# Performance work log

Measured on AMD Instinct MI355X. Metric: run time of the kernel, lower is better.

The kernel has to match this reference:

```python
import jax, jax.numpy as jnp
import numpy as np

GROUP = 128

def _dequant(q, s, z):
    # q: [O, K] int4 values in [0,16); s,z: [O, K//GROUP]
    O, K = q.shape
    qg = q.reshape(O, K // GROUP, GROUP)
    w = (qg - z[:, :, None]).astype(s.dtype) * s[:, :, None]
    return w.reshape(O, K)

def setup_inputs() -> dict:
    key = jax.random.key(0)
    ks = jax.random.split(key, 7)
    H, I = 4096, 14336
    x = jax.random.normal(ks[0], (2, 2048, H), jnp.float32)
    q_up = jax.random.randint(ks[1], (I, H), 0, 16, jnp.int32)
    s_up = (jax.random.uniform(ks[2], (I, H // GROUP), jnp.float32) * 0.02 + 1e-3)
    z_up = jax.random.randint(ks[3], (I, H // GROUP), 0, 16, jnp.int32)
    q_down = jax.random.randint(ks[4], (H, I), 0, 16, jnp.int32)
    s_down = (jax.random.uniform(ks[5], (H, I // GROUP), jnp.float32) * 0.02 + 1e-3)
    z_down = jax.random.randint(ks[6], (H, I // GROUP), 0, 16, jnp.int32)
    return {"x": x, "q_up": q_up, "s_up": s_up, "z_up": z_up,
            "q_down": q_down, "s_down": s_down, "z_down": z_down}

def reference(x, q_up, s_up, z_up, q_down, s_down, z_down):
    # up_proj: W4A16 dequant + GEMM, weight layout [out, in] like nn.Linear
    w_up = _dequant(q_up, s_up, z_up)        # [I, H]
    h = jnp.einsum('bsh,ih->bsi', x, w_up)   # [B, S, I]
    # NemotronH 'relu2' activation: relu(h)^2
    a = jnp.square(jax.nn.relu(h))
    w_down = _dequant(q_down, s_down, z_down)  # [H, I]
    y = jnp.einsum('bsi,hi->bsh', a, w_down)   # [B, S, H]
    return y
```

## Files before the change

kernel.cpp:

```cpp
#include <hip/hip_runtime.h>
#include <stdint.h>

typedef unsigned short u16;
typedef __attribute__((ext_vector_type(4))) float f32x4;
typedef __attribute__((ext_vector_type(8))) __bf16 bf16x8;
typedef __attribute__((ext_vector_type(8))) unsigned short u16x8;

__device__ __forceinline__ u16 f2bf(float f) {
  unsigned u = __builtin_bit_cast(unsigned, f);
  u = (u + 0x7fffu + ((u >> 16) & 1u)) >> 16;
  return (u16)u;
}

typedef __attribute__((address_space(1))) const void gvoid_t;
typedef __attribute__((address_space(3))) void lvoid_t;

__device__ __forceinline__ void gload_lds16(const void* g, void* l) {
  __builtin_amdgcn_global_load_lds((gvoid_t*)g, (lvoid_t*)l, 16, 0, 0);
}

__global__ __launch_bounds__(256)
void dequant_kernel(const int* __restrict__ q, const float* __restrict__ s,
                    const int* __restrict__ z, u16* __restrict__ w, int K) {
  const int row = blockIdx.y;
  const int k = (blockIdx.x * 256 + threadIdx.x) << 3;
  const int ng = K >> 7;
  const int g = k >> 7;
  const float sv = s[(size_t)row * ng + g];
  const float zv = (float)z[(size_t)row * ng + g];
  const int4* qp = (const int4*)(q + (size_t)row * K + k);
  const int4 a = qp[0], b = qp[1];
  u16x8 o;
  o[0] = f2bf(((float)a.x - zv) * sv);
  o[1] = f2bf(((float)a.y - zv) * sv);
  o[2] = f2bf(((float)a.z - zv) * sv);
  o[3] = f2bf(((float)a.w - zv) * sv);
  o[4] = f2bf(((float)b.x - zv) * sv);
  o[5] = f2bf(((float)b.y - zv) * sv);
  o[6] = f2bf(((float)b.z - zv) * sv);
  o[7] = f2bf(((float)b.w - zv) * sv);
  *reinterpret_cast<u16x8*>(w + (size_t)row * K + k) = o;
}

__global__ __launch_bounds__(256)
void cvt_kernel(const float* __restrict__ in, u16* __restrict__ out) {
  const size_t i = ((size_t)blockIdx.x * 256 + threadIdx.x) << 3;
  const float4* p = (const float4*)(in + i);
  const float4 a = p[0], b = p[1];
  u16x8 o;
  o[0] = f2bf(a.x); o[1] = f2bf(a.y); o[2] = f2bf(a.z); o[3] = f2bf(a.w);
  o[4] = f2bf(b.x); o[5] = f2bf(b.y); o[6] = f2bf(b.z); o[7] = f2bf(b.w);
  *reinterpret_cast<u16x8*>(out + i) = o;
}

template<bool RELU2>
__global__ __launch_bounds__(512, 2)
void gemm256(const u16* __restrict__ Ap, const u16* __restrict__ Bp,
             void* __restrict__ Cptr, int M, int N, int K) {
  __shared__ __align__(16) u16 As[2][256][64];
  __shared__ __align__(16) u16 Bs[2][256][64];
  const int tid = threadIdx.x;
  const int lane = tid & 63;
  const int wid = tid >> 6;
  const int wr = wid >> 2, wc = wid & 3;

  const int nbx = N >> 8;
  const int nwg = gridDim.x;
  int bid = blockIdx.x;
  bid = (bid & 7) * (nwg >> 3) + (bid >> 3);
  const int m0 = (bid / nbx) << 8;
  const int n0 = (bid % nbx) << 8;

  const int srow = tid >> 3;
  const int scol = tid & 7;
  const int lr = lane & 15;
  const int lk = (lane >> 4) << 3;
  const int xorc = (lr & 7) << 3;

  f32x4 acc[8][4] = {};
  bf16x8 a1[4], a2[4], a3[4], a4[4], b1[4], b2[4];

  const int nk = K >> 6;

#define STG_A(bufi, h, kt) do { _Pragma("unroll") \
  for (int l_ = 0; l_ < 2; ++l_) { \
    const int r_ = (h) * 128 + l_ * 64 + srow; \
    gload_lds16(Ap + (size_t)(m0 + r_) * K + (size_t)((kt) << 6) + ((scol ^ (srow & 7)) << 3), \
                &As[bufi][r_][scol << 3]); } } while (0)
#define STG_B(bufi, h, kt) do { _Pragma("unroll") \
  for (int l_ = 0; l_ < 2; ++l_) { \
    const int r_ = (h) * 128 + l_ * 64 + srow; \
    gload_lds16(Bp + (size_t)(n0 + r_) * K + (size_t)((kt) << 6) + ((scol ^ (srow & 7)) << 3), \
                &Bs[bufi][r_][scol << 3]); } } while (0)
#define RD_A(bufi, ks, half, dst) do { _Pragma("unroll") \
  for (int i_ = 0; i_ < 4; ++i_) { \
    const int row_ = wr * 128 + ((half) * 4 + i_) * 16 + lr; \
    dst[i_] = *reinterpret_cast<const bf16x8*>(&As[bufi][row_][((ks) * 32 + lk) ^ xorc]); } } while (0)
#define RD_B(bufi, ks, dst) do { _Pragma("unroll") \
  for (int j_ = 0; j_ < 4; ++j_) { \
    const int row_ = wc * 64 + j_ * 16 + lr; \
    dst[j_] = *reinterpret_cast<const bf16x8*>(&Bs[bufi][row_][((ks) * 32 + lk) ^ xorc]); } } while (0)
#define MFMA16(ASET, BSET, I0) do { _Pragma("unroll") \
  for (int i_ = 0; i_ < 4; ++i_) { _Pragma("unroll") \
    for (int j_ = 0; j_ < 4; ++j_) \
      acc[(I0) + i_][j_] = __builtin_amdgcn_mfma_f32_16x16x32_bf16( \
        ASET[i_], BSET[j_], acc[(I0) + i_][j_], 0, 0, 0); } } while (0)
#define BAR() do { asm volatile("" ::: "memory"); __builtin_amdgcn_s_barrier(); \
  asm volatile("" ::: "memory"); } while (0)
#define VMGATE() asm volatile("s_waitcnt vmcnt(0)" ::: "memory")
#define TILE(p, q, ktn) do { \
  RD_B(p, 0, b1); RD_A(p, 0, 0, a1); RD_A(p, 0, 1, a2); \
  STG_A(q, 0, ktn); STG_A(q, 1, ktn); \
  BAR(); __builtin_amdgcn_s_setprio(1); MFMA16(a1, b1, 0); __builtin_amdgcn_s_setprio(0); BAR(); \
  RD_A(p, 1, 0, a3); RD_B(p, 1, b2); \
  STG_B(q, 0, ktn); STG_B(q, 1, ktn); \
  BAR(); __builtin_amdgcn_s_setprio(1); MFMA16(a2, b1, 4); __builtin_amdgcn_s_setprio(0); BAR(); \
  RD_A(p, 1, 1, a4); \
  BAR(); __builtin_amdgcn_s_setprio(1); MFMA16(a3, b2, 0); __builtin_amdgcn_s_setprio(0); BAR(); \
  VMGATE(); \
  BAR(); __builtin_amdgcn_s_setprio(1); MFMA16(a4, b2, 4); __builtin_amdgcn_s_setprio(0); BAR(); \
} while (0)

  STG_A(0, 0, 0); STG_A(0, 1, 0);
  STG_B(0, 0, 0); STG_B(0, 1, 0);
  VMGATE();
  BAR();

  const int nit = nk >> 1;
  for (int it = 0; it < nit; ++it) {
    const int t1 = 2 * it + 1;
    int t2 = 2 * it + 2; if (t2 >= nk) t2 = 0;
    TILE(0, 1, t1);
    TILE(1, 0, t2);
  }

  const int crow = (lane >> 4) << 2;
  const int ccol = lane & 15;
#pragma unroll
  for (int i = 0; i < 8; ++i) {
#pragma unroll
    for (int j = 0; j < 4; ++j) {
#pragma unroll
      for (int q = 0; q < 4; ++q) {
        const int m = m0 + wr * 128 + i * 16 + crow + q;
        const int n = n0 + wc * 64 + j * 16 + ccol;
        const float v = acc[i][j][q];
        if constexpr (RELU2) {
          const float r = fmaxf(v, 0.f);
          ((u16*)Cptr)[(size_t)m * N + n] = f2bf(r * r);
        } else {
          ((float*)Cptr)[(size_t)m * N + n] = v;
        }
      }
    }
  }
#undef STG_A
#undef STG_B
#undef RD_A
#undef RD_B
#undef MFMA16
#undef BAR
#undef VMGATE
#undef TILE
}

extern "C" void kernel_launch(void* const* d_in, const int* in_sizes, int n_in,
                              void* d_out, int out_size, void* d_ws, size_t ws_size,
                              hipStream_t stream) {
  const float* x    = (const float*)d_in[0];
  const int*   q_up = (const int*)d_in[1];
  const float* s_up = (const float*)d_in[2];
  const int*   z_up = (const int*)d_in[3];
  const int*   q_dn = (const int*)d_in[4];
  const float* s_dn = (const float*)d_in[5];
  const int*   z_dn = (const int*)d_in[6];
  float* y = (float*)d_out;

  const int H = 4096, I = 14336;
  const int M = in_sizes[0] / H;

  const size_t wbytes = (size_t)I * H * 2;
  const size_t abytes = (size_t)M * I * 2;
  const size_t xbytes = (size_t)M * H * 2;
  u16* wbuf = (u16*)d_ws;
  u16* abuf = (u16*)((char*)d_ws + wbytes);
  u16* xbf  = (u16*)((char*)d_ws + wbytes + abytes);
  if (ws_size < wbytes + abytes + xbytes) return;

  dequant_kernel<<<dim3(H / 8 / 256, I), 256, 0, stream>>>(q_up, s_up, z_up, wbuf, H);
  cvt_kernel<<<dim3((int)(((size_t)M * H) >> 11)), 256, 0, stream>>>(x, xbf);
  gemm256<true><<<dim3((M / 256) * (I / 256)), 512, 0, stream>>>(xbf, wbuf, abuf, M, I, H);
  dequant_kernel<<<dim3(I / 8 / 256, H), 256, 0, stream>>>(q_dn, s_dn, z_dn, wbuf, I);
  gemm256<false><<<dim3((M / 256) * (H / 256)), 512, 0, stream>>>(abuf, wbuf, y, M, H, I);
}
```

Measured before the change: 1.068 ms.

## Restructure GEMM main loop into staggered four-phase pipeline with partial vmcnt gates

The GEMM main loop now issues the A-tile global-to-LDS loads one full k-tile ahead of the B-tile loads. Each k-tile is split into four phases, each guarded by an lgkmcnt wait and a sched_barrier. The full vmcnt(0) drain is replaced by vmcnt(4), so some global loads stay in flight across tile boundaries. The aim is to hide global-load latency behind MFMA work and to give the compiler's scheduling a fixed order. The risk is correctness around LDS buffer reuse: A data for tile t+2 is written into a buffer that other waves may still be reading, which depends on the barrier placement.

```diff
diff --git a/kernel.cpp b/kernel.cpp
--- a/kernel.cpp
+++ b/kernel.cpp
@@ -107,32 +107,38 @@
         ASET[i_], BSET[j_], acc[(I0) + i_][j_], 0, 0, 0); } } while (0)
 #define BAR() do { asm volatile("" ::: "memory"); __builtin_amdgcn_s_barrier(); \
   asm volatile("" ::: "memory"); } while (0)
-#define VMGATE() asm volatile("s_waitcnt vmcnt(0)" ::: "memory")
-#define TILE(p, q, ktn) do { \
-  RD_B(p, 0, b1); RD_A(p, 0, 0, a1); RD_A(p, 0, 1, a2); \
-  STG_A(q, 0, ktn); STG_A(q, 1, ktn); \
-  BAR(); __builtin_amdgcn_s_setprio(1); MFMA16(a1, b1, 0); __builtin_amdgcn_s_setprio(0); BAR(); \
-  RD_A(p, 1, 0, a3); RD_B(p, 1, b2); \
-  STG_B(q, 0, ktn); STG_B(q, 1, ktn); \
-  BAR(); __builtin_amdgcn_s_setprio(1); MFMA16(a2, b1, 4); __builtin_amdgcn_s_setprio(0); BAR(); \
-  RD_A(p, 1, 1, a4); \
-  BAR(); __builtin_amdgcn_s_setprio(1); MFMA16(a3, b2, 0); __builtin_amdgcn_s_setprio(0); BAR(); \
-  VMGATE(); \
-  BAR(); __builtin_amdgcn_s_setprio(1); MFMA16(a4, b2, 4); __builtin_amdgcn_s_setprio(0); BAR(); \
-} while (0)
+#define PH(Q) do { BAR(); \
+  asm volatile("s_waitcnt lgkmcnt(0)" ::: "memory"); \
+  __builtin_amdgcn_sched_barrier(0); \
+  __builtin_amdgcn_s_setprio(1); Q; __builtin_amdgcn_s_setprio(0); \
+  BAR(); } while (0)
+#define PH_GATE(Q) do { BAR(); \
+  asm volatile("s_waitcnt lgkmcnt(0)" ::: "memory"); \
+  __builtin_amdgcn_sched_barrier(0); \
+  __builtin_amdgcn_s_setprio(1); Q; __builtin_amdgcn_s_setprio(0); \
+  asm volatile("s_waitcnt vmcnt(4)" ::: "memory"); \
+  BAR(); } while (0)
+#define TILE4(p, S1, S2, S3, S4) do { \
+  RD_A(p, 0, 0, a1); RD_B(p, 0, b1); S1; PH(MFMA16(a1, b1, 0)); \
+  RD_A(p, 0, 1, a2); RD_A(p, 1, 1, a4); RD_A(p, 1, 0, a3); S2; PH(MFMA16(a2, b1, 4)); \
+  RD_B(p, 1, b2); S3; PH(MFMA16(a4, b2, 4)); \
+  S4; PH_GATE(MFMA16(a3, b2, 0)); } while (0)
 
   STG_A(0, 0, 0); STG_A(0, 1, 0);
   STG_B(0, 0, 0); STG_B(0, 1, 0);
-  VMGATE();
+  STG_A(1, 0, 1); STG_A(1, 1, 1);
+  asm volatile("s_waitcnt vmcnt(4)" ::: "memory");
   BAR();
 
   const int nit = nk >> 1;
   for (int it = 0; it < nit; ++it) {
     const int t1 = 2 * it + 1;
-    int t2 = 2 * it + 2; if (t2 >= nk) t2 = 0;
-    TILE(0, 1, t1);
-    TILE(1, 0, t2);
+    int t2 = 2 * it + 2; if (t2 >= nk) t2 -= nk;
+    int t3 = 2 * it + 3; if (t3 >= nk) t3 -= nk;
+    TILE4(0, STG_B(1, 0, t1), STG_B(1, 1, t1), STG_A(0, 0, t2), STG_A(0, 1, t2));
+    TILE4(1, STG_B(0, 0, t2), STG_B(0, 1, t2), STG_A(1, 0, t3), STG_A(1, 1, t3));
   }
+  asm volatile("s_waitcnt vmcnt(0)" ::: "memory");
 
   const int crow = (lane >> 4) << 2;
   const int ccol = lane & 15;
@@ -160,8 +166,9 @@
 #undef RD_B
 #undef MFMA16
 #undef BAR
-#undef VMGATE
-#undef TILE
+#undef PH
+#undef PH_GATE
+#undef TILE4
 }
 
 extern "C" void kernel_launch(void* const* d_in, const int* in_sizes, int n_in,
```

Result: no change. 1.084 ms (+1.4%).
